# Performance work log

Hardware: AMD Instinct MI355X
Metric: run time of the kernel (lower is better)

## Reference

```python
import jax, jax.numpy as jnp
import numpy as np
import math

B, L, D = 2, 4096, 1024
K = D // 4


def _rotor(angles):
    # angles: [..., 6] -> scalar part s: [...], bivector part: [..., 6]
    mag = jnp.maximum(jnp.linalg.norm(angles, axis=-1), 1e-8)
    s = jnp.cos(mag)
    biv = (jnp.sin(mag) / mag)[..., None] * angles
    return s, biv


def _apply_rotor(s, biv, v):
    # s: [...], biv: [..., 6] (e12,e13,e14,e23,e24,e34), v: [..., 4]
    t12, t13, t14, t23, t24, t34 = (biv[..., i] for i in range(6))
    v1, v2, v3, v4 = (v[..., i] for i in range(4))
    s2 = s * s
    ts = 2.0 * s
    v1n = v1 * (s2 - t12 * t12 - t13 * t13 - t14 * t14) + ts * (v2 * t12 + v3 * t13 + v4 * t14)
    v2n = v2 * (s2 - t12 * t12 - t23 * t23 - t24 * t24) + ts * (-v1 * t12 + v3 * t23 + v4 * t24)
    v3n = v3 * (s2 - t13 * t13 - t23 * t23 - t34 * t34) + ts * (-v1 * t13 - v2 * t23 + v4 * t34)
    v4n = v4 * (s2 - t14 * t14 - t24 * t24 - t34 * t34) + ts * (-v1 * t14 - v2 * t24 - v3 * t34)
    return jnp.stack([v1n, v2n, v3n, v4n], axis=-1)


def _forward(x, wk1, bk1, wk2, bk2, wq1, bq1, wq2, bq2, wv, bv, ln_g, ln_b, wo, bo):
    b, l, d = x.shape
    k = d // 4
    gelu = lambda t: jax.nn.gelu(t, approximate=False)  # torch nn.GELU default = exact
    half_pi = math.pi / 2
    key_angles = (jnp.tanh(gelu(x @ wk1 + bk1) @ wk2 + bk2) * half_pi).reshape(b, l, k, 6)
    query_angles = (jnp.tanh(gelu(x @ wq1 + bq1) @ wq2 + bq2) * half_pi).reshape(b, l, k, 6)
    value = (x @ wv + bv).reshape(b, l, k, 4)
    ks, kb = _rotor(key_angles)
    qs, qb = _rotor(query_angles)
    rotated_value = _apply_rotor(ks, kb, value)          # [B,L,K,4]
    memory = jnp.cumsum(rotated_value, axis=1)            # running sum over sequence
    retrieved = _apply_rotor(qs, -qb, memory)             # reversed query rotor
    retrieved = retrieved.reshape(b, l, d)
    norm = jnp.sqrt(jnp.arange(1, l + 1, dtype=x.dtype))[None, :, None]
    r = retrieved / norm
    # LayerNorm (eps=1e-5) then Linear
    mu = jnp.mean(r, axis=-1, keepdims=True)
    var = jnp.mean((r - mu) ** 2, axis=-1, keepdims=True)
    rn = (r - mu) / jnp.sqrt(var + 1e-5) * ln_g + ln_b
    return x + rn @ wo + bo


def setup_inputs() -> dict:
    key = jax.random.key(0)
    ks = jax.random.split(key, 8)
    lin = lambda k, fi, fo: (jax.random.normal(k, (fi, fo), jnp.float32) * 0.02)
    return {
        "x": jax.random.normal(ks[0], (B, L, D), jnp.float32),
        "wk1": lin(ks[1], D, D), "bk1": jnp.zeros((D,), jnp.float32),
        "wk2": lin(ks[2], D, K * 6), "bk2": jnp.zeros((K * 6,), jnp.float32),
        "wq1": lin(ks[3], D, D), "bq1": jnp.zeros((D,), jnp.float32),
        "wq2": lin(ks[4], D, K * 6), "bq2": jnp.zeros((K * 6,), jnp.float32),
        "wv": lin(ks[5], D, D), "bv": jnp.zeros((D,), jnp.float32),
        "ln_g": jnp.ones((D,), jnp.float32), "ln_b": jnp.zeros((D,), jnp.float32),
        "wo": lin(ks[6], D, D), "bo": jnp.zeros((D,), jnp.float32),
    }


def reference(x, wk1, bk1, wk2, bk2, wq1, bq1, wq2, bq2, wv, bv, ln_g, ln_b, wo, bo):
    return _forward(x, wk1, bk1, wk2, bk2, wq1, bq1, wq2, bq2, wv, bv, ln_g, ln_b, wo, bo)
```

## Files before the change

### kernel.cpp

```cpp
#include <hip/hip_runtime.h>
#include <hip/hip_bf16.h>
#include <math.h>

#define D_DIM 1024
#define L_DIM 4096
#define B_DIM 2
#define K_DIM 256
#define N6    1536
#define M_ROWS 8192
#define CHUNKS 256
#define CHUNK_LEN 16
#define HALF_PI 1.57079632679489662f

typedef __attribute__((ext_vector_type(8))) short short8;
typedef __attribute__((ext_vector_type(4))) float f32x4;
typedef unsigned short us;

__device__ __forceinline__ void gload_lds16(const void* g, void* l) {
    __builtin_amdgcn_global_load_lds(
        (const __attribute__((address_space(1))) unsigned int*)g,
        (__attribute__((address_space(3))) unsigned int*)l,
        16, 0, 0);
}
__device__ __forceinline__ float bf2f(us u) {
    union { unsigned int i; float f; } c; c.i = ((unsigned int)u) << 16; return c.f;
}
__device__ __forceinline__ us f2bf(float v) {
    __hip_bfloat16 h = __float2bfloat16(v);
    return *(us*)&h;
}
__device__ __forceinline__ float tanh_fast(float x) {
    return 1.0f - 2.0f / (1.0f + __expf(2.0f * x));
}
__device__ __forceinline__ float gelu_fast(float x) {
    return x / (1.0f + __expf(-1.5957691216057308f * x * (1.0f + 0.044715f * x * x)));
}

__device__ __forceinline__ void rotor_from_angles(const float a[6], float& s, float b[6]) {
    float m2 = a[0]*a[0] + a[1]*a[1] + a[2]*a[2] + a[3]*a[3] + a[4]*a[4] + a[5]*a[5];
    float mag = fmaxf(sqrtf(m2), 1e-8f);
    s = __cosf(mag);
    float f = __sinf(mag) / mag;
    #pragma unroll
    for (int i = 0; i < 6; ++i) b[i] = f * a[i];
}
__device__ __forceinline__ void apply_rotor(float s, const float b[6], const float v[4], float o[4]) {
    float t12 = b[0], t13 = b[1], t14 = b[2], t23 = b[3], t24 = b[4], t34 = b[5];
    float v1 = v[0], v2 = v[1], v3 = v[2], v4 = v[3];
    float s2 = s * s;
    float ts = 2.0f * s;
    o[0] = v1 * (s2 - t12*t12 - t13*t13 - t14*t14) + ts * ( v2*t12 + v3*t13 + v4*t14);
    o[1] = v2 * (s2 - t12*t12 - t23*t23 - t24*t24) + ts * (-v1*t12 + v3*t23 + v4*t24);
    o[2] = v3 * (s2 - t13*t13 - t23*t23 - t34*t34) + ts * (-v1*t13 - v2*t23 + v4*t34);
    o[3] = v4 * (s2 - t14*t14 - t24*t24 - t34*t34) + ts * (-v1*t14 - v2*t24 - v3*t34);
}

__global__ __launch_bounds__(256)
void pack_b4(const float* __restrict__ w0, const float* __restrict__ w1,
             const float* __restrict__ w2, const float* __restrict__ w3,
             us* __restrict__ o0, us* __restrict__ o1,
             us* __restrict__ o2, us* __restrict__ o3, int Kd, int N)
{
    const float* W = (blockIdx.z == 0) ? w0 : (blockIdx.z == 1) ? w1 : (blockIdx.z == 2) ? w2 : w3;
    us* O = (blockIdx.z == 0) ? o0 : (blockIdx.z == 1) ? o1 : (blockIdx.z == 2) ? o2 : o3;
    if (W == nullptr) return;
    int nf = blockIdx.x;
    int kt = blockIdx.y * 4 + (threadIdx.x >> 6);
    int l = threadIdx.x & 63;
    int n = nf * 16 + (l & 15);
    int k0 = kt * 32 + (l >> 4) * 8;
    union { us u[8]; uint4 v; } pk;
    #pragma unroll
    for (int j = 0; j < 8; ++j)
        pk.u[j] = f2bf(W[(size_t)(k0 + j) * N + n]);
    *(uint4*)(O + ((size_t)nf * (Kd >> 5) + kt) * 512 + l * 8) = pk.v;
}

__global__ __launch_bounds__(256)
void cvt_bf16_kernel(const float* __restrict__ in, us* __restrict__ out)
{
    size_t i = ((size_t)blockIdx.x * 256 + threadIdx.x) * 8;
    float4 v0 = *(const float4*)(in + i);
    float4 v1 = *(const float4*)(in + i + 4);
    union { us u[8]; uint4 v; } pk;
    pk.u[0] = f2bf(v0.x); pk.u[1] = f2bf(v0.y); pk.u[2] = f2bf(v0.z); pk.u[3] = f2bf(v0.w);
    pk.u[4] = f2bf(v1.x); pk.u[5] = f2bf(v1.y); pk.u[6] = f2bf(v1.z); pk.u[7] = f2bf(v1.w);
    *(uint4*)(out + i) = pk.v;
}

__device__ __forceinline__ int xcd_swz(int bid, int nwg) {
    int cpx = nwg >> 3;
    return (bid & 7) * cpx + (bid >> 3);
}

#define GBAR()  do { __builtin_amdgcn_s_barrier(); __builtin_amdgcn_sched_barrier(0); } while (0)

__device__ __forceinline__ void gemm128_core(
    const us* __restrict__ Ab, const us* __restrict__ Bp, int Kd, int bn,
    short* lds, f32x4 (&acc)[4][4])
{
    const int tid = threadIdx.x;
    const int l = tid & 63, w = tid >> 6;
    const int wr = w >> 1, wc = w & 1;
    const int fr = l & 15, fq = l >> 4;
    const int nkt = Kd >> 5;

    #pragma unroll
    for (int i = 0; i < 4; ++i)
        #pragma unroll
        for (int j = 0; j < 4; ++j)
            acc[i][j] = (f32x4){0.f, 0.f, 0.f, 0.f};

    const us* bptr[4];
    #pragma unroll
    for (int ni = 0; ni < 4; ++ni)
        bptr[ni] = Bp + ((size_t)((bn >> 4) + wc * 4 + ni) * nkt) * 512 + l * 8;

    const int sr = tid >> 2, su = tid & 3;
    const int slu = su ^ ((sr >> 1) & 3);
    const us* gA0 = Ab + (size_t)sr * Kd + slu * 8;
    const us* gA1 = gA0 + (size_t)64 * Kd;

    const int swu = (fq ^ ((fr >> 1) & 3)) * 8;
    const int arow = (wr * 64 + fr) * 32 + swu;

    gload_lds16(gA0,      lds + tid * 8);
    gload_lds16(gA1,      lds + 2048 + tid * 8);
    gload_lds16(gA0 + 32, lds + 4096 + tid * 8);
    gload_lds16(gA1 + 32, lds + 6144 + tid * 8);
    gload_lds16(gA0 + 64, lds + 8192 + tid * 8);
    gload_lds16(gA1 + 64, lds + 10240 + tid * 8);
    asm volatile("s_waitcnt vmcnt(4)" ::: "memory");
    short8 bA[4], bB[4];
    #pragma unroll
    for (int ni = 0; ni < 4; ++ni) bA[ni] = *(const short8*)(bptr[ni]);
    #pragma unroll
    for (int ni = 0; ni < 4; ++ni) bB[ni] = *(const short8*)(bptr[ni] + 512);
    GBAR();

    for (int t = 0; t < nkt; t += 2) {
        {
            const int cb = (t % 3) * 4096;
            const int sb = ((t + 2) % 3) * 4096;
            const int tp = (t + 2 < nkt) ? (t + 2) : (nkt - 1);
            short8 a[4];
            #pragma unroll
            for (int mi = 0; mi < 4; ++mi)
                a[mi] = *(const short8*)(lds + cb + arow + mi * 512);
            gload_lds16(gA0 + tp * 32, lds + sb + tid * 8);
            gload_lds16(gA1 + tp * 32, lds + sb + 2048 + tid * 8);
            __builtin_amdgcn_s_setprio(1);
            #pragma unroll
            for (int mi = 0; mi < 4; ++mi)
                #pragma unroll
                for (int ni = 0; ni < 4; ++ni)
                    acc[mi][ni] = __builtin_amdgcn_mfma_f32_16x16x32_bf16(bA[ni], a[mi], acc[mi][ni], 0, 0, 0);
            __builtin_amdgcn_sched_barrier(0);
            __builtin_amdgcn_s_setprio(0);
            #pragma unroll
            for (int ni = 0; ni < 4; ++ni)
                bA[ni] = *(const short8*)(bptr[ni] + (size_t)tp * 512);
            asm volatile("s_waitcnt vmcnt(6)" ::: "memory");
            GBAR();
        }
        {
            const int t1 = t + 1;
            const int cb = (t1 % 3) * 4096;
            const int sb = ((t1 + 2) % 3) * 4096;
            const int tp = (t1 + 2 < nkt) ? (t1 + 2) : (nkt - 1);
            short8 a[4];
            #pragma unroll
            for (int mi = 0; mi < 4; ++mi)
                a[mi] = *(const short8*)(lds + cb + arow + mi * 512);
            gload_lds16(gA0 + tp * 32, lds + sb + tid * 8);
            gload_lds16(gA1 + tp * 32, lds + sb + 2048 + tid * 8);
            __builtin_amdgcn_s_setprio(1);
            #pragma unroll
            for (int mi = 0; mi < 4; ++mi)
                #pragma unroll
                for (int ni = 0; ni < 4; ++ni)
                    acc[mi][ni] = __builtin_amdgcn_mfma_f32_16x16x32_bf16(bB[ni], a[mi], acc[mi][ni], 0, 0, 0);
            __builtin_amdgcn_sched_barrier(0);
            __builtin_amdgcn_s_setprio(0);
            #pragma unroll
            for (int ni = 0; ni < 4; ++ni)
                bB[ni] = *(const short8*)(bptr[ni] + (size_t)tp * 512);
            asm volatile("s_waitcnt vmcnt(6)" ::: "memory");
            GBAR();
        }
    }
}

__global__ __launch_bounds__(256, 3)
void gemm_fused3(const us* __restrict__ xb,
                 const us* __restrict__ w0p, const us* __restrict__ w1p, const us* __restrict__ w2p,
                 const float* __restrict__ b0, const float* __restrict__ b1, const float* __restrict__ b2,
                 us* __restrict__ o0, us* __restrict__ o1, us* __restrict__ o2)
{
    __shared__ short lds[12288];
    const int wg = xcd_swz(blockIdx.x, 1536);
    const int bm = (wg / 24) * 128;
    const int col = wg % 24;
    const int r = col >> 3;
    const int bn = (col & 7) * 128;
    const us* Bp = (r == 0) ? w0p : (r == 1) ? w1p : w2p;
    const float* bias = (r == 0) ? b0 : (r == 1) ? b1 : b2;
    us* outp = (r == 0) ? o0 : (r == 1) ? o1 : o2;
    f32x4 acc[4][4];
    gemm128_core(xb + (size_t)bm * D_DIM, Bp, D_DIM, bn, lds, acc);
    const int l = threadIdx.x & 63, w = threadIdx.x >> 6;
    const int wr = w >> 1, wc = w & 1, fr = l & 15, fq = l >> 4;
    #pragma unroll
    for (int mi = 0; mi < 4; ++mi) {
        int row = bm + wr * 64 + mi * 16 + fr;
        #pragma unroll
        for (int ni = 0; ni < 4; ++ni) {
            int c0 = bn + wc * 64 + ni * 16 + fq * 4;
            float4 bs = *(const float4*)(bias + c0);
            float v0 = acc[mi][ni][0] + bs.x, v1 = acc[mi][ni][1] + bs.y;
            float v2 = acc[mi][ni][2] + bs.z, v3 = acc[mi][ni][3] + bs.w;
            if (r < 2) { v0 = gelu_fast(v0); v1 = gelu_fast(v1); v2 = gelu_fast(v2); v3 = gelu_fast(v3); }
            ushort4 pk; pk.x = f2bf(v0); pk.y = f2bf(v1); pk.z = f2bf(v2); pk.w = f2bf(v3);
            *(ushort4*)(outp + (size_t)row * D_DIM + c0) = pk;
        }
    }
}

__global__ __launch_bounds__(256, 3)
void gemm_angles(const us* __restrict__ Hk, const us* __restrict__ Hq,
                 const us* __restrict__ wk2p, const us* __restrict__ wq2p,
                 const float* __restrict__ bk2, const float* __restrict__ bq2,
                 us* __restrict__ ak, us* __restrict__ aq)
{
    __shared__ short lds[12288];
    const int wg = xcd_swz(blockIdx.x, 1536);
    const int z = wg / 768;
    const int rem = wg % 768;
    const int bm = (rem / 12) * 128;
    const int bn = (rem % 12) * 128;
    const us* A  = z ? Hq : Hk;
    const us* Bp = z ? wq2p : wk2p;
    const float* bias = z ? bq2 : bk2;
    us* outp = z ? aq : ak;
    f32x4 acc[4][4];
    gemm128_core(A + (size_t)bm * D_DIM, Bp, D_DIM, bn, lds, acc);
    const int l = threadIdx.x & 63, w = threadIdx.x >> 6;
    const int wr = w >> 1, wc = w & 1, fr = l & 15, fq = l >> 4;
    #pragma unroll
    for (int mi = 0; mi < 4; ++mi) {
        int row = bm + wr * 64 + mi * 16 + fr;
        #pragma unroll
        for (int ni = 0; ni < 4; ++ni) {
            int c0 = bn + wc * 64 + ni * 16 + fq * 4;
            float4 bs = *(const float4*)(bias + c0);
            ushort4 pk;
            pk.x = f2bf(tanh_fast(acc[mi][ni][0] + bs.x) * HALF_PI);
            pk.y = f2bf(tanh_fast(acc[mi][ni][1] + bs.y) * HALF_PI);
            pk.z = f2bf(tanh_fast(acc[mi][ni][2] + bs.z) * HALF_PI);
            pk.w = f2bf(tanh_fast(acc[mi][ni][3] + bs.w) * HALF_PI);
            *(ushort4*)(outp + (size_t)row * N6 + c0) = pk;
        }
    }
}

__global__ __launch_bounds__(256, 3)
void gemm_final(const us* __restrict__ rn, const us* __restrict__ wop,
                const float* __restrict__ bo, const float* __restrict__ x,
                float* __restrict__ out)
{
    __shared__ short lds[12288];
    const int wg = xcd_swz(blockIdx.x, 512);
    const int bm = (wg / 8) * 128;
    const int bn = (wg % 8) * 128;
    f32x4 acc[4][4];
    gemm128_core(rn + (size_t)bm * D_DIM, wop, D_DIM, bn, lds, acc);
    const int l = threadIdx.x & 63, w = threadIdx.x >> 6;
    const int wr = w >> 1, wc = w & 1, fr = l & 15, fq = l >> 4;
    #pragma unroll
    for (int mi = 0; mi < 4; ++mi) {
        int row = bm + wr * 64 + mi * 16 + fr;
        #pragma unroll
        for (int ni = 0; ni < 4; ++ni) {
            int c0 = bn + wc * 64 + ni * 16 + fq * 4;
            size_t off = (size_t)row * D_DIM + c0;
            float4 bs = *(const float4*)(bo + c0);
            float4 rx = *(const float4*)(x + off);
            float4 o;
            o.x = acc[mi][ni][0] + bs.x + rx.x;
            o.y = acc[mi][ni][1] + bs.y + rx.y;
            o.z = acc[mi][ni][2] + bs.z + rx.z;
            o.w = acc[mi][ni][3] + bs.w + rx.w;
            *(float4*)(out + off) = o;
        }
    }
}

__global__ __launch_bounds__(256)
void rot_chunk_sum(us* __restrict__ value, const us* __restrict__ ak,
                   float4* __restrict__ sums)
{
    int bc = blockIdx.x;
    int b = bc >> 8, c = bc & 255;
    int k = threadIdx.x;
    float4 acc = make_float4(0.f, 0.f, 0.f, 0.f);
    size_t row0 = (size_t)b * L_DIM + c * CHUNK_LEN;
    for (int i = 0; i < CHUNK_LEN; ++i) {
        size_t row = row0 + i;
        ushort4 uv = *(const ushort4*)(value + row * D_DIM + k * 4);
        const unsigned int* ap = (const unsigned int*)(ak + row * N6 + k * 6);
        unsigned int a0 = ap[0], a1 = ap[1], a2 = ap[2];
        float a[6] = { bf2f(a0 & 0xffff), bf2f(a0 >> 16), bf2f(a1 & 0xffff),
                       bf2f(a1 >> 16), bf2f(a2 & 0xffff), bf2f(a2 >> 16) };
        float s, bb[6];
        rotor_from_angles(a, s, bb);
        float v[4] = {bf2f(uv.x), bf2f(uv.y), bf2f(uv.z), bf2f(uv.w)}, o[4];
        apply_rotor(s, bb, v, o);
        ushort4 pkr;
        pkr.x = f2bf(o[0]); pkr.y = f2bf(o[1]); pkr.z = f2bf(o[2]); pkr.w = f2bf(o[3]);
        *(ushort4*)(value + row * D_DIM + k * 4) = pkr;
        acc.x += bf2f(pkr.x); acc.y += bf2f(pkr.y); acc.z += bf2f(pkr.z); acc.w += bf2f(pkr.w);
    }
    sums[(size_t)bc * 256 + k] = acc;
}

__global__ __launch_bounds__(256)
void scan_chunks_kernel(const float4* __restrict__ sums, float4* __restrict__ carry)
{
    int b = blockIdx.x >> 8;
    int k = blockIdx.x & 255;
    int c = threadIdx.x;
    __shared__ float4 sh[CHUNKS];
    float4 v = sums[((size_t)(b * CHUNKS + c)) * 256 + k];
    sh[c] = v;
    __syncthreads();
    for (int off = 1; off < CHUNKS; off <<= 1) {
        float4 t = make_float4(0.f, 0.f, 0.f, 0.f);
        if (c >= off) t = sh[c - off];
        __syncthreads();
        v.x += t.x; v.y += t.y; v.z += t.z; v.w += t.w;
        sh[c] = v;
        __syncthreads();
    }
    float4 ex = make_float4(0.f, 0.f, 0.f, 0.f);
    if (c > 0) ex = sh[c - 1];
    carry[((size_t)(b * CHUNKS + c)) * 256 + k] = ex;
}

__global__ __launch_bounds__(256)
void scan_apply_ln(const us* __restrict__ value, const us* __restrict__ aq,
                   const float4* __restrict__ carry,
                   const float* __restrict__ g, const float* __restrict__ bta,
                   us* __restrict__ rn)
{
    int bc = blockIdx.x;
    int b = bc >> 8, c = bc & 255;
    int k = threadIdx.x;
    int wv = k >> 6, lane = k & 63;
    float4 run = carry[(size_t)bc * 256 + k];
    float4 gv = *(const float4*)(g + k * 4);
    float4 bv = *(const float4*)(bta + k * 4);
    __shared__ float reds[4], redq[4];
    for (int i = 0; i < CHUNK_LEN; ++i) {
        int l = c * CHUNK_LEN + i;
        size_t row = (size_t)b * L_DIM + l;
        ushort4 uv = *(const ushort4*)(value + row * D_DIM + k * 4);
        run.x += bf2f(uv.x); run.y += bf2f(uv.y); run.z += bf2f(uv.z); run.w += bf2f(uv.w);
        const unsigned int* aqp = (const unsigned int*)(aq + row * N6 + k * 6);
        unsigned int qa0 = aqp[0], qa1 = aqp[1], qa2 = aqp[2];
        float aq6[6] = { bf2f(qa0 & 0xffff), bf2f(qa0 >> 16), bf2f(qa1 & 0xffff),
                         bf2f(qa1 >> 16), bf2f(qa2 & 0xffff), bf2f(qa2 >> 16) };
        float qs, qb[6];
        rotor_from_angles(aq6, qs, qb);
        #pragma unroll
        for (int t = 0; t < 6; ++t) qb[t] = -qb[t];
        float mem[4] = {run.x, run.y, run.z, run.w}, o2[4];
        apply_rotor(qs, qb, mem, o2);
        float inv = rsqrtf((float)(l + 1));
        o2[0] *= inv; o2[1] *= inv; o2[2] *= inv; o2[3] *= inv;
        float sm = o2[0] + o2[1] + o2[2] + o2[3];
        float qm = o2[0]*o2[0] + o2[1]*o2[1] + o2[2]*o2[2] + o2[3]*o2[3];
        #pragma unroll
        for (int off = 1; off < 64; off <<= 1) {
            sm += __shfl_xor(sm, off);
            qm += __shfl_xor(qm, off);
        }
        if (lane == 0) { reds[wv] = sm; redq[wv] = qm; }
        __syncthreads();
        sm = reds[0] + reds[1] + reds[2] + reds[3];
        qm = redq[0] + redq[1] + redq[2] + redq[3];
        float mu = sm * (1.0f / 1024.0f);
        float var = qm * (1.0f / 1024.0f) - mu * mu;
        float rstd = rsqrtf(var + 1e-5f);
        ushort4 pk;
        pk.x = f2bf((o2[0] - mu) * rstd * gv.x + bv.x);
        pk.y = f2bf((o2[1] - mu) * rstd * gv.y + bv.y);
        pk.z = f2bf((o2[2] - mu) * rstd * gv.z + bv.z);
        pk.w = f2bf((o2[3] - mu) * rstd * gv.w + bv.w);
        *(ushort4*)(rn + row * D_DIM + k * 4) = pk;
        __syncthreads();
    }
}

extern "C" void kernel_launch(void* const* d_in, const int* in_sizes, int n_in,
                              void* d_out, int out_size, void* d_ws, size_t ws_size,
                              hipStream_t stream)
{
    const float* x   = (const float*)d_in[0];
    const float* wk1 = (const float*)d_in[1];
    const float* bk1 = (const float*)d_in[2];
    const float* wk2 = (const float*)d_in[3];
    const float* bk2 = (const float*)d_in[4];
    const float* wq1 = (const float*)d_in[5];
    const float* bq1 = (const float*)d_in[6];
    const float* wq2 = (const float*)d_in[7];
    const float* bq2 = (const float*)d_in[8];
    const float* wv  = (const float*)d_in[9];
    const float* bv  = (const float*)d_in[10];
    const float* lng = (const float*)d_in[11];
    const float* lnb = (const float*)d_in[12];
    const float* wo  = (const float*)d_in[13];
    const float* bo  = (const float*)d_in[14];
    float* out = (float*)d_out;

    char* ws = (char*)d_ws;
    us* xb    = (us*)(ws);
    us* Hk    = (us*)(ws + (16ull  << 20));
    us* Hq    = (us*)(ws + (32ull  << 20));
    us* val   = (us*)(ws + (48ull  << 20));
    us* ak    = (us*)(ws + (64ull  << 20));
    us* aq    = (us*)(ws + (88ull  << 20));
    float4* sums  = (float4*)(ws + (112ull << 20));
    float4* carry = (float4*)(ws + (114ull << 20));
    us* wk1p  = (us*)(ws + (116ull << 20));
    us* wq1p  = (us*)(ws + (118ull << 20));
    us* wvp   = (us*)(ws + (120ull << 20));
    us* wop   = (us*)(ws + (122ull << 20));
    us* wk2p  = (us*)(ws + (124ull << 20));
    us* wq2p  = (us*)(ws + (127ull << 20));
    us* rn    = xb;

    dim3 blk(256);
    pack_b4<<<dim3(D_DIM / 16, D_DIM / 128, 4), blk, 0, stream>>>(
        wk1, wq1, wv, wo, wk1p, wq1p, wvp, wop, D_DIM, D_DIM);
    pack_b4<<<dim3(N6 / 16, D_DIM / 128, 2), blk, 0, stream>>>(
        wk2, wq2, nullptr, nullptr, wk2p, wq2p, nullptr, nullptr, D_DIM, N6);
    cvt_bf16_kernel<<<dim3(M_ROWS * D_DIM / (256 * 8)), blk, 0, stream>>>(x, xb);

    gemm_fused3<<<dim3(1536), blk, 0, stream>>>(
        xb, wk1p, wq1p, wvp, bk1, bq1, bv, Hk, Hq, val);
    gemm_angles<<<dim3(1536), blk, 0, stream>>>(
        Hk, Hq, wk2p, wq2p, bk2, bq2, ak, aq);
    rot_chunk_sum<<<dim3(B_DIM * CHUNKS), blk, 0, stream>>>(val, ak, sums);
    scan_chunks_kernel<<<dim3(B_DIM * K_DIM), blk, 0, stream>>>(sums, carry);
    scan_apply_ln<<<dim3(B_DIM * CHUNKS), blk, 0, stream>>>(val, aq, carry, lng, lnb, rn);
    gemm_final<<<dim3(512), blk, 0, stream>>>(rn, wop, bo, x, out);
}
```

Measured before the change: 230.3 us.

## Give each wave a private LDS ring for A tiles and drop block barriers

Restructures the shared GEMM core so each wave streams its own 64-row slice of A into a private triple-buffered LDS ring. The workgroup-wide s_barrier calls go away and only per-wave vmcnt waits remain. The two waves that share the same rows now each load their own copy, which doubles A traffic from L2 and doubles LDS per block to 48KB. That may cut occupancy headroom and raise memory pressure.

```diff
diff --git a/kernel.cpp b/kernel.cpp
--- a/kernel.cpp
+++ b/kernel.cpp
@@ -93,8 +93,6 @@
     return (bid & 7) * cpx + (bid >> 3);
 }
 
-#define GBAR()  do { __builtin_amdgcn_s_barrier(); __builtin_amdgcn_sched_barrier(0); } while (0)
-
 __device__ __forceinline__ void gemm128_core(
     const us* __restrict__ Ab, const us* __restrict__ Bp, int Kd, int bn,
     short* lds, f32x4 (&acc)[4][4])
@@ -116,39 +114,47 @@
     for (int ni = 0; ni < 4; ++ni)
         bptr[ni] = Bp + ((size_t)((bn >> 4) + wc * 4 + ni) * nkt) * 512 + l * 8;
 
-    const int sr = tid >> 2, su = tid & 3;
-    const int slu = su ^ ((sr >> 1) & 3);
-    const us* gA0 = Ab + (size_t)sr * Kd + slu * 8;
-    const us* gA1 = gA0 + (size_t)64 * Kd;
+    short* ring = lds + w * 6144;
+    const us* Aw = Ab + (size_t)(wr * 64) * Kd;
+
+    const us* gA[4];
+    int dsto[4];
+    #pragma unroll
+    for (int j = 0; j < 4; ++j) {
+        int idx = l + j * 64;
+        int row = idx >> 2, u = idx & 3;
+        int lu = u ^ ((row >> 1) & 3);
+        gA[j] = Aw + (size_t)row * Kd + lu * 8;
+        dsto[j] = idx * 8;
+    }
 
     const int swu = (fq ^ ((fr >> 1) & 3)) * 8;
-    const int arow = (wr * 64 + fr) * 32 + swu;
-
-    gload_lds16(gA0,      lds + tid * 8);
-    gload_lds16(gA1,      lds + 2048 + tid * 8);
-    gload_lds16(gA0 + 32, lds + 4096 + tid * 8);
-    gload_lds16(gA1 + 32, lds + 6144 + tid * 8);
-    gload_lds16(gA0 + 64, lds + 8192 + tid * 8);
-    gload_lds16(gA1 + 64, lds + 10240 + tid * 8);
-    asm volatile("s_waitcnt vmcnt(4)" ::: "memory");
+    const int arow = fr * 32 + swu;
+
+    #pragma unroll
+    for (int j = 0; j < 4; ++j) gload_lds16(gA[j],      ring + dsto[j]);
+    #pragma unroll
+    for (int j = 0; j < 4; ++j) gload_lds16(gA[j] + 32, ring + 2048 + dsto[j]);
     short8 bA[4], bB[4];
     #pragma unroll
     for (int ni = 0; ni < 4; ++ni) bA[ni] = *(const short8*)(bptr[ni]);
     #pragma unroll
     for (int ni = 0; ni < 4; ++ni) bB[ni] = *(const short8*)(bptr[ni] + 512);
-    GBAR();
+    asm volatile("s_waitcnt vmcnt(12)" ::: "memory");
+    __builtin_amdgcn_sched_barrier(0);
 
     for (int t = 0; t < nkt; t += 2) {
         {
-            const int cb = (t % 3) * 4096;
-            const int sb = ((t + 2) % 3) * 4096;
+            const int cb = (t % 3) * 2048;
+            const int sb = ((t + 2) % 3) * 2048;
             const int tp = (t + 2 < nkt) ? (t + 2) : (nkt - 1);
             short8 a[4];
             #pragma unroll
             for (int mi = 0; mi < 4; ++mi)
-                a[mi] = *(const short8*)(lds + cb + arow + mi * 512);
-            gload_lds16(gA0 + tp * 32, lds + sb + tid * 8);
-            gload_lds16(gA1 + tp * 32, lds + sb + 2048 + tid * 8);
+                a[mi] = *(const short8*)(ring + cb + mi * 512 + arow);
+            #pragma unroll
+            for (int j = 0; j < 4; ++j)
+                gload_lds16(gA[j] + tp * 32, ring + sb + dsto[j]);
             __builtin_amdgcn_s_setprio(1);
             #pragma unroll
             for (int mi = 0; mi < 4; ++mi)
@@ -160,20 +166,21 @@
             #pragma unroll
             for (int ni = 0; ni < 4; ++ni)
                 bA[ni] = *(const short8*)(bptr[ni] + (size_t)tp * 512);
-            asm volatile("s_waitcnt vmcnt(6)" ::: "memory");
-            GBAR();
+            asm volatile("s_waitcnt vmcnt(12)" ::: "memory");
+            __builtin_amdgcn_sched_barrier(0);
         }
         {
             const int t1 = t + 1;
-            const int cb = (t1 % 3) * 4096;
-            const int sb = ((t1 + 2) % 3) * 4096;
+            const int cb = (t1 % 3) * 2048;
+            const int sb = ((t1 + 2) % 3) * 2048;
             const int tp = (t1 + 2 < nkt) ? (t1 + 2) : (nkt - 1);
             short8 a[4];
             #pragma unroll
             for (int mi = 0; mi < 4; ++mi)
-                a[mi] = *(const short8*)(lds + cb + arow + mi * 512);
-            gload_lds16(gA0 + tp * 32, lds + sb + tid * 8);
-            gload_lds16(gA1 + tp * 32, lds + sb + 2048 + tid * 8);
+                a[mi] = *(const short8*)(ring + cb + mi * 512 + arow);
+            #pragma unroll
+            for (int j = 0; j < 4; ++j)
+                gload_lds16(gA[j] + tp * 32, ring + sb + dsto[j]);
             __builtin_amdgcn_s_setprio(1);
             #pragma unroll
             for (int mi = 0; mi < 4; ++mi)
@@ -185,8 +192,8 @@
             #pragma unroll
             for (int ni = 0; ni < 4; ++ni)
                 bB[ni] = *(const short8*)(bptr[ni] + (size_t)tp * 512);
-            asm volatile("s_waitcnt vmcnt(6)" ::: "memory");
-            GBAR();
+            asm volatile("s_waitcnt vmcnt(12)" ::: "memory");
+            __builtin_amdgcn_sched_barrier(0);
         }
     }
 }
@@ -197,7 +204,7 @@
                  const float* __restrict__ b0, const float* __restrict__ b1, const float* __restrict__ b2,
                  us* __restrict__ o0, us* __restrict__ o1, us* __restrict__ o2)
 {
-    __shared__ short lds[12288];
+    __shared__ short lds[24576];
     const int wg = xcd_swz(blockIdx.x, 1536);
     const int bm = (wg / 24) * 128;
     const int col = wg % 24;
@@ -232,7 +239,7 @@
                  const float* __restrict__ bk2, const float* __restrict__ bq2,
                  us* __restrict__ ak, us* __restrict__ aq)
 {
-    __shared__ short lds[12288];
+    __shared__ short lds[24576];
     const int wg = xcd_swz(blockIdx.x, 1536);
     const int z = wg / 768;
     const int rem = wg % 768;
@@ -268,7 +275,7 @@
                 const float* __restrict__ bo, const float* __restrict__ x,
                 float* __restrict__ out)
 {
-    __shared__ short lds[12288];
+    __shared__ short lds[24576];
     const int wg = xcd_swz(blockIdx.x, 512);
     const int bm = (wg / 8) * 128;
     const int bn = (wg % 8) * 128;
```

Measured after the change: 269.3 us. 16.9% more time.
